# Optimization experiments

Measured on AMD Instinct MI355X. Metric: run time of the kernel, lower is better.

The kernel has to match this reference:

```python
import jax, jax.numpy as jnp
import numpy as np

B, T, H, OUT, L = 125, 512, 512, 1024, 2


def _rnn_layer(xs, w_ih, w_hh, b_ih, b_hh):
    # xs: [B, T, H_in] -> scan over time with tanh recurrence
    xs_t = jnp.swapaxes(xs, 0, 1)  # [T, B, H_in]
    h0 = jnp.zeros((xs.shape[0], w_hh.shape[0]), dtype=xs.dtype)

    def step(h, x_t):
        h = jnp.tanh(x_t @ w_ih.T + b_ih + h @ w_hh.T + b_hh)
        return h, h

    h_last, hs = jax.lax.scan(step, h0, xs_t)
    return jnp.swapaxes(hs, 0, 1), h_last  # [B, T, H], [B, H]


def setup_inputs() -> dict:
    key = jax.random.key(0)
    ks = jax.random.split(key, 8)
    s = 1.0 / np.sqrt(H)
    x = jax.random.normal(ks[0], (B, T, H), dtype=jnp.float32)
    w_ih = jax.random.uniform(ks[1], (L, H, H), jnp.float32, -s, s)
    w_hh = jax.random.uniform(ks[2], (L, H, H), jnp.float32, -s, s)
    b_ih = jax.random.uniform(ks[3], (L, H), jnp.float32, -s, s)
    b_hh = jax.random.uniform(ks[4], (L, H), jnp.float32, -s, s)
    fc_w = jax.random.uniform(ks[5], (OUT, H), jnp.float32, -s, s)
    fc_b = jax.random.uniform(ks[6], (OUT,), jnp.float32, -s, s)
    return {"x": x, "w_ih": w_ih, "w_hh": w_hh, "b_ih": b_ih,
            "b_hh": b_hh, "fc_w": fc_w, "fc_b": fc_b}


def reference(x, w_ih, w_hh, b_ih, b_hh, fc_w, fc_b):
    h = x
    finals = []
    for l in range(L):  # small fixed layer loop
        h, h_last = _rnn_layer(h, w_ih[l], w_hh[l], b_ih[l], b_hh[l])
        finals.append(h_last)
    hidden = jnp.stack(finals, axis=0)  # [L, B, H]
    out = h.reshape(-1, H) @ fc_w.T + fc_b  # [B*T, OUT]
    return out, hidden
```

## Files before the change

kernel.cpp:

```cpp
#include <hip/hip_runtime.h>
#include <hip/hip_bf16.h>
#include <cstdint>

typedef short short8 __attribute__((ext_vector_type(8)));
typedef float f32x4 __attribute__((ext_vector_type(4)));
typedef uint32_t u32x2 __attribute__((ext_vector_type(2)));
typedef unsigned short u16;

#define DEVINL __device__ __forceinline__

DEVINL u16 f32_to_bf16(float f) {
  uint32_t u = __builtin_bit_cast(uint32_t, f);
  u += 0x7FFFu + ((u >> 16) & 1u);
  return (u16)(u >> 16);
}
DEVINL float bf16_to_f32(u16 b) {
  return __builtin_bit_cast(float, ((uint32_t)b) << 16);
}
DEVINL f32x4 mfma16(short8 a, short8 b, f32x4 c) {
  return __builtin_amdgcn_mfma_f32_16x16x32_bf16(a, b, c, 0, 0, 0);
}
DEVINL float tanh_e2(float x) {
  float e = __builtin_amdgcn_exp2f(x * 2.88539008177793f);
  return 1.f - __fdividef(2.f, 1.f + e);
}
DEVINL uint32_t cvt_pk_bf16(float lo, float hi) {
  uint32_t r;
  asm("v_cvt_pk_bf16_f32 %0, %1, %2" : "=v"(r) : "v"(lo), "v"(hi));
  return r;
}

__global__ void conv_bf16(const float* __restrict__ src, u16* __restrict__ dst, long n) {
  long i = ((long)blockIdx.x * blockDim.x + threadIdx.x) * 4;
  long stride = (long)gridDim.x * blockDim.x * 4;
  for (; i < n; i += stride) {
    float4 v = *(const float4*)(src + i);
    uint64_t p = (uint64_t)f32_to_bf16(v.x)
               | ((uint64_t)f32_to_bf16(v.y) << 16)
               | ((uint64_t)f32_to_bf16(v.z) << 32)
               | ((uint64_t)f32_to_bf16(v.w) << 48);
    *(uint64_t*)(dst + i) = p;
  }
}

__global__ void prep_bias(const float* __restrict__ bih, const float* __restrict__ bhh,
                          float* __restrict__ b1, float* __restrict__ b2) {
  int i = threadIdx.x;
  b1[i] = bih[i]       + bhh[i];
  b2[i] = bih[512 + i] + bhh[512 + i];
}

DEVINL void rec_window(char* LDS, int g, const u16* __restrict__ Whh,
                       const u16* __restrict__ U, u16* __restrict__ Hout,
                       float* __restrict__ hidden, u16* __restrict__ hstate, int win) {
  const int tid  = threadIdx.x;
  const int lane = tid & 63;
  const int w    = tid >> 6;
  const int q    = lane >> 4;
  const int r16  = lane & 15;
  const int t0   = win << 6;

  short8 wreg[3][16];
#pragma unroll
  for (int tt = 0; tt < 3; ++tt)
#pragma unroll
    for (int kk = 0; kk < 16; ++kk)
      wreg[tt][kk] = *(const short8*)(Whh + (size_t)(w * 64 + tt * 16 + r16) * 512 + kk * 32 + q * 8);

#pragma unroll
  for (int kk = 0; kk < 16; ++kk) {
    short8 v = *(const short8*)(Whh + (size_t)(w * 64 + 48 + r16) * 512 + kk * 32 + q * 8);
    *(short8*)(LDS + w * 16384 + kk * 1024 + q * 256 + r16 * 16) = v;
  }

  if (win == 0) {
    short8 z = {0, 0, 0, 0, 0, 0, 0, 0};
    *(short8*)(LDS + 131072 + tid * 32)      = z;
    *(short8*)(LDS + 131072 + tid * 32 + 16) = z;
  } else {
    short8 a = *(const short8*)(hstate + (size_t)g * 8192 + tid * 16);
    short8 b = *(const short8*)(hstate + (size_t)g * 8192 + tid * 16 + 8);
    *(short8*)(LDS + 131072 + tid * 32)      = a;
    *(short8*)(LDS + 131072 + tid * 32 + 16) = b;
  }

  uint32_t rd  = 131072 + q * 256 + r16 * 16;
  uint32_t wrb = 147456 + w * 2048 + (q >> 1) * 256 + r16 * 16 + (q & 1) * 8;
  const uint32_t wlb = w * 16384 + q * 256 + r16 * 16;
  const int jb = w * 64 + q * 4;
  const char* Ub = (const char*)U;
  const uint32_t ubase = (uint32_t)(g * 512 + tid) * 32;
  char* Hc = (char*)Hout;
  uint32_t hoff = (uint32_t)(g * 16 + r16) * 524288u + (uint32_t)jb * 2u + (uint32_t)t0 * 1024u;

  short8 u  = *(const short8*)(Ub + ubase + (uint32_t)t0 * 131072u);
  short8 u2 = *(const short8*)(Ub + ubase + (uint32_t)t0 * 131072u + 16);
  __syncthreads();

  for (int t = t0; t < t0 + 64; ++t) {
    f32x4 D0, D1, D2, D3;
#pragma unroll
    for (int rg = 0; rg < 4; ++rg) {
      D0[rg] = bf16_to_f32((u16)u[rg]);
      D1[rg] = bf16_to_f32((u16)u[rg + 4]);
      D2[rg] = bf16_to_f32((u16)u2[rg]);
      D3[rg] = bf16_to_f32((u16)u2[rg + 4]);
    }
    {
      uint32_t off = ubase + (uint32_t)((t + 1 <= 511) ? (t + 1) : 511) * 131072u;
      u  = *(const short8*)(Ub + off);
      u2 = *(const short8*)(Ub + off + 16);
    }
#pragma unroll
    for (int kk = 0; kk < 16; ++kk) {
      short8 hf = *(const short8*)(LDS + rd + kk * 1024);
      short8 wl = *(const short8*)(LDS + wlb + kk * 1024);
      D0 = mfma16(wreg[0][kk], hf, D0);
      D1 = mfma16(wreg[1][kk], hf, D1);
      D2 = mfma16(wreg[2][kk], hf, D2);
      D3 = mfma16(wl, hf, D3);
    }
#define EPI_TILE(Dt, tt) { \
    float e0 = tanh_e2(Dt[0]), e1 = tanh_e2(Dt[1]); \
    float e2 = tanh_e2(Dt[2]), e3 = tanh_e2(Dt[3]); \
    u32x2 pk; pk[0] = cvt_pk_bf16(e0, e1); pk[1] = cvt_pk_bf16(e2, e3); \
    *(u32x2*)(LDS + wrb + ((tt) >> 1) * 1024 + ((tt) & 1) * 512) = pk; \
    *(u32x2*)(Hc + hoff + (tt) * 32) = pk; \
  }
    EPI_TILE(D0, 0); EPI_TILE(D1, 1); EPI_TILE(D2, 2); EPI_TILE(D3, 3);
#undef EPI_TILE
    hoff += 1024;

    rd ^= 16384; wrb ^= 16384;
    asm volatile("s_waitcnt lgkmcnt(0)" ::: "memory");
    __builtin_amdgcn_s_barrier();
    asm volatile("" ::: "memory");
  }

  {
    short8 a = *(const short8*)(LDS + 131072 + tid * 32);
    short8 b = *(const short8*)(LDS + 131072 + tid * 32 + 16);
    *(short8*)(hstate + (size_t)g * 8192 + tid * 16)     = a;
    *(short8*)(hstate + (size_t)g * 8192 + tid * 16 + 8) = b;
  }

  if (win == 7) {
    int b = g * 16 + r16;
    if (b < 125) {
      uint32_t fwr = 131072 + w * 2048 + (q >> 1) * 256 + r16 * 16 + (q & 1) * 8;
#pragma unroll
      for (int tt = 0; tt < 4; ++tt) {
        u32x2 pk = *(const u32x2*)(LDS + fwr + (tt >> 1) * 1024 + (tt & 1) * 512);
        float4 v;
        v.x = __builtin_bit_cast(float, pk[0] << 16);
        v.y = __builtin_bit_cast(float, pk[0] & 0xFFFF0000u);
        v.z = __builtin_bit_cast(float, pk[1] << 16);
        v.w = __builtin_bit_cast(float, pk[1] & 0xFFFF0000u);
        *(float4*)(hidden + (size_t)b * 512 + jb + tt * 16) = v;
      }
    }
  }
}

template <int MR, int AF32, int FRAG>
DEVINL void gemm_tile(char* LDS, const void* __restrict__ Ap,
                      const u16* __restrict__ B, const float* __restrict__ bias,
                      void* __restrict__ out, int brow, int bcol, int N) {
  u16* lA = (u16*)LDS;
  u16* lB = (u16*)(LDS + 16384);
  const int tid  = threadIdx.x;
  const int lane = tid & 63;
  const int wave = tid >> 6;
  const int wr = wave >> 2;
  const int wc = wave & 3;
  const int q   = lane >> 4;
  const int r16 = lane & 15;
  const int MT = MR / 32;

  f32x4 acc[MT][2];
#pragma unroll
  for (int i = 0; i < MT; ++i)
#pragma unroll
    for (int j = 0; j < 2; ++j) acc[i][j] = (f32x4){0.f, 0.f, 0.f, 0.f};

  for (int kt = 0; kt < 8; ++kt) {
    if (AF32) {
#pragma unroll
      for (int s = 0; s < 2; ++s) {
        int c   = tid * 2 + s;
        int row = c >> 3;
        int seg = c & 7;
        const float* src = (const float*)Ap + (size_t)(brow + row) * 512 + kt * 64 + seg * 8;
        float4 a0 = *(const float4*)(src);
        float4 a1 = *(const float4*)(src + 4);
        u32x2 p0, p1;
        p0[0] = cvt_pk_bf16(a0.x, a0.y); p0[1] = cvt_pk_bf16(a0.z, a0.w);
        p1[0] = cvt_pk_bf16(a1.x, a1.y); p1[1] = cvt_pk_bf16(a1.z, a1.w);
        int dsw = (seg * 16) ^ ((row & 7) << 4);
        *(u32x2*)((char*)lA + row * 128 + dsw)     = p0;
        *(u32x2*)((char*)lA + row * 128 + (dsw ^ 8)) = p1;
      }
    } else {
      const int CH = MR / 64;
#pragma unroll
      for (int s = 0; s < CH; ++s) {
        int c   = tid * CH + s;
        int row = c >> 3;
        int cb  = (c & 7) * 16;
        int dsw = cb ^ ((row & 7) << 4);
        short8 va = *(const short8*)((const u16*)Ap + (size_t)(brow + row) * 512 + kt * 64 + (cb >> 1));
        *(short8*)((char*)lA + row * 128 + dsw) = va;
      }
    }
#pragma unroll
    for (int s = 0; s < 2; ++s) {
      int c   = tid * 2 + s;
      int row = c >> 3;
      int cb  = (c & 7) * 16;
      int dsw = cb ^ ((row & 7) << 4);
      short8 vb = *(const short8*)(B + (size_t)(bcol + row) * 512 + kt * 64 + (cb >> 1));
      *(short8*)((char*)lB + row * 128 + dsw) = vb;
    }
    __syncthreads();
#pragma unroll
    for (int kk = 0; kk < 2; ++kk) {
      short8 af[MT], bfr[2];
#pragma unroll
      for (int mt = 0; mt < MT; ++mt) {
        int row = wr * (MR / 2) + mt * 16 + r16;
        int byt = (kk * 64 + q * 16) ^ ((row & 7) << 4);
        af[mt] = *(const short8*)((const char*)lA + row * 128 + byt);
      }
#pragma unroll
      for (int nt = 0; nt < 2; ++nt) {
        int row = wc * 32 + nt * 16 + r16;
        int byt = (kk * 64 + q * 16) ^ ((row & 7) << 4);
        bfr[nt] = *(const short8*)((const char*)lB + row * 128 + byt);
      }
#pragma unroll
      for (int mt = 0; mt < MT; ++mt)
#pragma unroll
        for (int nt = 0; nt < 2; ++nt)
          acc[mt][nt] = mfma16(af[mt], bfr[nt], acc[mt][nt]);
    }
    __syncthreads();
  }

#pragma unroll
  for (int mt = 0; mt < MT; ++mt) {
#pragma unroll
    for (int nt = 0; nt < 2; ++nt) {
      int jc = bcol + wc * 32 + nt * 16 + r16;
      float bv = bias[jc];
      if (!FRAG) {
#pragma unroll
        for (int rg = 0; rg < 4; ++rg) {
          int mg = brow + wr * (MR / 2) + mt * 16 + q * 4 + rg;
          ((float*)out)[(size_t)mg * N + jc] = acc[mt][nt][rg] + bv;
        }
      } else {
        int tidc    = (jc >> 6) * 64 + ((jc >> 2) & 3) * 16;
        int colpart = ((jc >> 4) & 3) * 4 + (jc & 3);
#pragma unroll
        for (int rg = 0; rg < 4; ++rg) {
          int mg = brow + wr * (MR / 2) + mt * 16 + q * 4 + rg;
          int bb = mg >> 9;
          int t2 = mg & 511;
          size_t idx = (((size_t)t2 * 8 + (bb >> 4)) * 512 + tidc + (bb & 15)) * 16 + colpart;
          ((u16*)out)[idx] = f32_to_bf16(acc[mt][nt][rg] + bv);
        }
      }
    }
  }
}

__attribute__((amdgpu_flat_work_group_size(512, 512), amdgpu_waves_per_eu(2, 2)))
__global__ void phase(const u16* __restrict__ Whh1, const u16* __restrict__ Whh2,
                      u16* __restrict__ U1, u16* __restrict__ U2,
                      u16* __restrict__ H1, u16* __restrict__ H2,
                      u16* __restrict__ hs1, u16* __restrict__ hs2,
                      const float* __restrict__ Xf, const u16* __restrict__ Wih1,
                      const u16* __restrict__ Wih2, const u16* __restrict__ FCW,
                      const float* __restrict__ b1, const float* __restrict__ b2,
                      const float* __restrict__ fcb,
                      float* __restrict__ outp, float* __restrict__ hid,
                      int rec1w, int rec2w, int njobs, int j0, int j1, int j2, int j3) {
  __shared__ char LDS[163840];
  const int bx = blockIdx.x;
  if (bx < 8) {
    if (rec1w >= 0) rec_window(LDS, bx, Whh1, U1, H1, hid, hs1, rec1w);
  } else if (bx < 16) {
    if (rec2w >= 0) rec_window(LDS, bx - 8, Whh2, U2, H2, hid + 64000, hs2, rec2w);
  } else if (njobs > 0) {
    const int widx = bx - 16;
    int jobs[4] = {j0, j1, j2, j3};
    int cnt[4], total = 0;
    for (int i = 0; i < njobs; ++i) { cnt[i] = ((jobs[i] >> 4) == 2) ? 1000 : 500; total += cnt[i]; }
    for (int tile = widx; tile < total; tile += 240) {
      int rem = tile, jj = 0;
      while (jj < njobs - 1 && rem >= cnt[jj]) { rem -= cnt[jj]; ++jj; }
      int kind = jobs[jj] >> 4, wn = jobs[jj] & 15;
      if (kind == 0)
        gemm_tile<128, 1, 1>(LDS, Xf, Wih1, b1, U1,
                             (rem >> 2) * 512 + wn * 128, (rem & 3) * 128, 512);
      else if (kind == 1)
        gemm_tile<64, 0, 1>(LDS, H1, Wih2, b2, U2,
                            (rem >> 2) * 512 + wn * 64, (rem & 3) * 128, 512);
      else
        gemm_tile<128, 0, 0>(LDS, H2, FCW, fcb, outp,
                             (rem >> 3) * 512 + wn * 128, (rem & 7) * 128, 1024);
    }
  }
}

#define J(k, w) ((k) * 16 + (w))

extern "C" void kernel_launch(void* const* d_in, const int* in_sizes, int n_in,
                              void* d_out, int out_size, void* d_ws, size_t ws_size,
                              hipStream_t stream) {
  const float* x   = (const float*)d_in[0];
  const float* wih = (const float*)d_in[1];
  const float* whh = (const float*)d_in[2];
  const float* bih = (const float*)d_in[3];
  const float* bhh = (const float*)d_in[4];
  const float* fcw = (const float*)d_in[5];
  const float* fcb = (const float*)d_in[6];

  char* ws = (char*)d_ws;
  float* outp = (float*)d_out;
  float* hid  = outp + 65536000;
  u16*   U1   = (u16*)d_out;

  u16* Wih1 = (u16*)(ws + 0);
  u16* Whh1 = (u16*)(ws + 524288);
  u16* Wih2 = (u16*)(ws + 1048576);
  u16* Whh2 = (u16*)(ws + 1572864);
  u16* FCW  = (u16*)(ws + 2097152);
  float* b1 = (float*)(ws + 3145728);
  float* b2 = b1 + 512;
  u16* hs1  = (u16*)(ws + 3276800);
  u16* hs2  = (u16*)(ws + 3407872);

  conv_bf16<<<256, 256, 0, stream>>>(wih,          Wih1, 262144L);
  conv_bf16<<<256, 256, 0, stream>>>(wih + 262144, Wih2, 262144L);
  conv_bf16<<<256, 256, 0, stream>>>(whh,          Whh1, 262144L);
  conv_bf16<<<256, 256, 0, stream>>>(whh + 262144, Whh2, 262144L);
  conv_bf16<<<512, 256, 0, stream>>>(fcw, FCW, 524288L);
  prep_bias<<<1, 512, 0, stream>>>(bih, bhh, b1, b2);

  if (ws_size >= 205520896ull) {
    u16* U2 = (u16*)(ws + 4194304);
    u16* H1 = (u16*)(ws + 71303168);
    u16* H2 = (u16*)(ws + 138412032);
#define PH(r1, r2, nj, a, b, c, d) \
    phase<<<256, 512, 0, stream>>>(Whh1, Whh2, U1, U2, H1, H2, hs1, hs2, x, \
                                   Wih1, Wih2, FCW, b1, b2, fcb, outp, hid, \
                                   r1, r2, nj, a, b, c, d)
    PH(-1, -1, 1, J(0,0), 0, 0, 0);
    PH( 0, -1, 3, J(0,1), J(0,2), J(0,3), 0);
    PH( 1, -1, 1, J(1,0), 0, 0, 0);
    PH( 2,  0, 1, J(1,1), 0, 0, 0);
    PH( 3,  1, 1, J(1,2), 0, 0, 0);
    PH( 4,  2, 1, J(1,3), 0, 0, 0);
    PH( 5,  3, 1, J(1,4), 0, 0, 0);
    PH( 6,  4, 1, J(1,5), 0, 0, 0);
    PH( 7,  5, 1, J(1,6), 0, 0, 0);
    PH(-1,  6, 3, J(1,7), J(2,0), J(2,1), 0);
    PH(-1,  7, 1, J(2,2), 0, 0, 0);
    PH(-1, -1, 1, J(2,3), 0, 0, 0);
#undef PH
  } else {
    u16* U2 = U1;
    u16* H1 = (u16*)(ws + 4194304);
    u16* H2 = H1;
#define PH(r1, r2, nj, a, b, c, d) \
    phase<<<256, 512, 0, stream>>>(Whh1, Whh2, U1, U2, H1, H2, hs1, hs2, x, \
                                   Wih1, Wih2, FCW, b1, b2, fcb, outp, hid, \
                                   r1, r2, nj, a, b, c, d)
    PH(-1, -1, 4, J(0,0), J(0,1), J(0,2), J(0,3));
    for (int w = 0; w < 8; ++w) PH(w, -1, 0, 0, 0, 0, 0);
    PH(-1, -1, 4, J(1,0), J(1,1), J(1,2), J(1,3));
    PH(-1, -1, 4, J(1,4), J(1,5), J(1,6), J(1,7));
    for (int w = 0; w < 8; ++w) PH(-1, w, 0, 0, 0, 0, 0);
    PH(-1, -1, 2, J(2,0), J(2,1), 0, 0);
    PH(-1, -1, 2, J(2,2), J(2,3), 0, 0);
#undef PH
  }

  (void)in_sizes; (void)n_in; (void)out_size;
}
```

Baseline: 1.720 ms.

## Pair row-tiles sharing B in layer-2 and FC GEMMs, fuse prep kernels

Replaces the templated GEMM tile with a dedicated float-input version for layer 1 and a paired version for the layer-2 input projection and the FC GEMM. The paired version loads one B tile and computes two 64-row A tiles from different batch blocks against it, so B traffic is shared. The FC GEMM is now split into 8 row windows instead of 4, rescheduling it across the last phases to better overlap with the layer-2 recurrence. The six weight/bias prep launches are merged into one kernel to cut launch overhead.

```diff
diff --git a/kernel.cpp b/kernel.cpp
--- a/kernel.cpp
+++ b/kernel.cpp
@@ -30,24 +30,34 @@
   return r;
 }
 
-__global__ void conv_bf16(const float* __restrict__ src, u16* __restrict__ dst, long n) {
-  long i = ((long)blockIdx.x * blockDim.x + threadIdx.x) * 4;
-  long stride = (long)gridDim.x * blockDim.x * 4;
-  for (; i < n; i += stride) {
-    float4 v = *(const float4*)(src + i);
-    uint64_t p = (uint64_t)f32_to_bf16(v.x)
-               | ((uint64_t)f32_to_bf16(v.y) << 16)
-               | ((uint64_t)f32_to_bf16(v.z) << 32)
-               | ((uint64_t)f32_to_bf16(v.w) << 48);
-    *(uint64_t*)(dst + i) = p;
-  }
-}
-
-__global__ void prep_bias(const float* __restrict__ bih, const float* __restrict__ bhh,
-                          float* __restrict__ b1, float* __restrict__ b2) {
-  int i = threadIdx.x;
-  b1[i] = bih[i]       + bhh[i];
-  b2[i] = bih[512 + i] + bhh[512 + i];
+__global__ void conv_all(const float* __restrict__ wih, const float* __restrict__ whh,
+                         const float* __restrict__ fcw, const float* __restrict__ bih,
+                         const float* __restrict__ bhh,
+                         u16* __restrict__ Wih1, u16* __restrict__ Wih2,
+                         u16* __restrict__ Whh1, u16* __restrict__ Whh2,
+                         u16* __restrict__ FCW, float* __restrict__ b1,
+                         float* __restrict__ b2) {
+  const int bx = blockIdx.x, tid = threadIdx.x;
+  if (bx == 1536) {
+    for (int i = tid; i < 512; i += 256) {
+      b1[i] = bih[i]       + bhh[i];
+      b2[i] = bih[512 + i] + bhh[512 + i];
+    }
+    return;
+  }
+  const float* src; u16* dst; int off;
+  if (bx < 256)       { src = wih;          dst = Wih1; off = bx; }
+  else if (bx < 512)  { src = wih + 262144; dst = Wih2; off = bx - 256; }
+  else if (bx < 768)  { src = whh;          dst = Whh1; off = bx - 512; }
+  else if (bx < 1024) { src = whh + 262144; dst = Whh2; off = bx - 768; }
+  else                { src = fcw;          dst = FCW;  off = bx - 1024; }
+  long i = (long)off * 1024 + tid * 4;
+  float4 v = *(const float4*)(src + i);
+  uint64_t p = (uint64_t)f32_to_bf16(v.x)
+             | ((uint64_t)f32_to_bf16(v.y) << 16)
+             | ((uint64_t)f32_to_bf16(v.z) << 32)
+             | ((uint64_t)f32_to_bf16(v.w) << 48);
+  *(uint64_t*)(dst + i) = p;
 }
 
 DEVINL void rec_window(char* LDS, int g, const u16* __restrict__ Whh,
@@ -162,10 +172,9 @@
   }
 }
 
-template <int MR, int AF32, int FRAG>
-DEVINL void gemm_tile(char* LDS, const void* __restrict__ Ap,
-                      const u16* __restrict__ B, const float* __restrict__ bias,
-                      void* __restrict__ out, int brow, int bcol, int N) {
+DEVINL void gemm_g1(char* LDS, const float* __restrict__ Ap, const u16* __restrict__ B,
+                    const float* __restrict__ bias, u16* __restrict__ out,
+                    int brow, int bcol) {
   u16* lA = (u16*)LDS;
   u16* lB = (u16*)(LDS + 16384);
   const int tid  = threadIdx.x;
@@ -175,42 +184,28 @@
   const int wc = wave & 3;
   const int q   = lane >> 4;
   const int r16 = lane & 15;
-  const int MT = MR / 32;
-
-  f32x4 acc[MT][2];
-#pragma unroll
-  for (int i = 0; i < MT; ++i)
+
+  f32x4 acc[4][2];
+#pragma unroll
+  for (int i = 0; i < 4; ++i)
 #pragma unroll
     for (int j = 0; j < 2; ++j) acc[i][j] = (f32x4){0.f, 0.f, 0.f, 0.f};
 
   for (int kt = 0; kt < 8; ++kt) {
-    if (AF32) {
-#pragma unroll
-      for (int s = 0; s < 2; ++s) {
-        int c   = tid * 2 + s;
-        int row = c >> 3;
-        int seg = c & 7;
-        const float* src = (const float*)Ap + (size_t)(brow + row) * 512 + kt * 64 + seg * 8;
-        float4 a0 = *(const float4*)(src);
-        float4 a1 = *(const float4*)(src + 4);
-        u32x2 p0, p1;
-        p0[0] = cvt_pk_bf16(a0.x, a0.y); p0[1] = cvt_pk_bf16(a0.z, a0.w);
-        p1[0] = cvt_pk_bf16(a1.x, a1.y); p1[1] = cvt_pk_bf16(a1.z, a1.w);
-        int dsw = (seg * 16) ^ ((row & 7) << 4);
-        *(u32x2*)((char*)lA + row * 128 + dsw)     = p0;
-        *(u32x2*)((char*)lA + row * 128 + (dsw ^ 8)) = p1;
-      }
-    } else {
-      const int CH = MR / 64;
-#pragma unroll
-      for (int s = 0; s < CH; ++s) {
-        int c   = tid * CH + s;
-        int row = c >> 3;
-        int cb  = (c & 7) * 16;
-        int dsw = cb ^ ((row & 7) << 4);
-        short8 va = *(const short8*)((const u16*)Ap + (size_t)(brow + row) * 512 + kt * 64 + (cb >> 1));
-        *(short8*)((char*)lA + row * 128 + dsw) = va;
-      }
+#pragma unroll
+    for (int s = 0; s < 2; ++s) {
+      int c   = tid * 2 + s;
+      int row = c >> 3;
+      int seg = c & 7;
+      const float* src = Ap + (size_t)(brow + row) * 512 + kt * 64 + seg * 8;
+      float4 a0 = *(const float4*)(src);
+      float4 a1 = *(const float4*)(src + 4);
+      u32x2 p0, p1;
+      p0[0] = cvt_pk_bf16(a0.x, a0.y); p0[1] = cvt_pk_bf16(a0.z, a0.w);
+      p1[0] = cvt_pk_bf16(a1.x, a1.y); p1[1] = cvt_pk_bf16(a1.z, a1.w);
+      int dsw = (seg * 16) ^ ((row & 7) << 4);
+      *(u32x2*)((char*)lA + row * 128 + dsw)       = p0;
+      *(u32x2*)((char*)lA + row * 128 + (dsw ^ 8)) = p1;
     }
 #pragma unroll
     for (int s = 0; s < 2; ++s) {
@@ -224,10 +219,10 @@
     __syncthreads();
 #pragma unroll
     for (int kk = 0; kk < 2; ++kk) {
-      short8 af[MT], bfr[2];
-#pragma unroll
-      for (int mt = 0; mt < MT; ++mt) {
-        int row = wr * (MR / 2) + mt * 16 + r16;
+      short8 af[4], bfr[2];
+#pragma unroll
+      for (int mt = 0; mt < 4; ++mt) {
+        int row = wr * 64 + mt * 16 + r16;
         int byt = (kk * 64 + q * 16) ^ ((row & 7) << 4);
         af[mt] = *(const short8*)((const char*)lA + row * 128 + byt);
       }
@@ -238,7 +233,7 @@
         bfr[nt] = *(const short8*)((const char*)lB + row * 128 + byt);
       }
 #pragma unroll
-      for (int mt = 0; mt < MT; ++mt)
+      for (int mt = 0; mt < 4; ++mt)
 #pragma unroll
         for (int nt = 0; nt < 2; ++nt)
           acc[mt][nt] = mfma16(af[mt], bfr[nt], acc[mt][nt]);
@@ -247,31 +242,129 @@
   }
 
 #pragma unroll
-  for (int mt = 0; mt < MT; ++mt) {
+  for (int mt = 0; mt < 4; ++mt) {
 #pragma unroll
     for (int nt = 0; nt < 2; ++nt) {
       int jc = bcol + wc * 32 + nt * 16 + r16;
       float bv = bias[jc];
-      if (!FRAG) {
-#pragma unroll
-        for (int rg = 0; rg < 4; ++rg) {
-          int mg = brow + wr * (MR / 2) + mt * 16 + q * 4 + rg;
-          ((float*)out)[(size_t)mg * N + jc] = acc[mt][nt][rg] + bv;
+      int tidc    = (jc >> 6) * 64 + ((jc >> 2) & 3) * 16;
+      int colpart = ((jc >> 4) & 3) * 4 + (jc & 3);
+#pragma unroll
+      for (int rg = 0; rg < 4; ++rg) {
+        int mg = brow + wr * 64 + mt * 16 + q * 4 + rg;
+        int bb = mg >> 9;
+        int t2 = mg & 511;
+        size_t idx = (((size_t)t2 * 8 + (bb >> 4)) * 512 + tidc + (bb & 15)) * 16 + colpart;
+        out[idx] = f32_to_bf16(acc[mt][nt][rg] + bv);
+      }
+    }
+  }
+}
+
+template <int FRAG>
+DEVINL void gemm_pair(char* LDS, const u16* __restrict__ Ap, int brow0, int brow1,
+                      const u16* __restrict__ B, const float* __restrict__ bias,
+                      void* __restrict__ out, int bcol, int N) {
+  u16* lB  = (u16*)LDS;
+  u16* lA0 = (u16*)(LDS + 16384);
+  u16* lA1 = (u16*)(LDS + 24576);
+  const int tid  = threadIdx.x;
+  const int lane = tid & 63;
+  const int wave = tid >> 6;
+  const int wr = wave >> 2;
+  const int wc = wave & 3;
+  const int q   = lane >> 4;
+  const int r16 = lane & 15;
+
+  f32x4 acc0[2][2], acc1[2][2];
+#pragma unroll
+  for (int i = 0; i < 2; ++i)
+#pragma unroll
+    for (int j = 0; j < 2; ++j) {
+      acc0[i][j] = (f32x4){0.f, 0.f, 0.f, 0.f};
+      acc1[i][j] = (f32x4){0.f, 0.f, 0.f, 0.f};
+    }
+
+  for (int kt = 0; kt < 8; ++kt) {
+#pragma unroll
+    for (int s = 0; s < 2; ++s) {
+      int c   = tid * 2 + s;
+      int row = c >> 3;
+      int cb  = (c & 7) * 16;
+      int dsw = cb ^ ((row & 7) << 4);
+      short8 vb = *(const short8*)(B + (size_t)(bcol + row) * 512 + kt * 64 + (cb >> 1));
+      *(short8*)((char*)lB + row * 128 + dsw) = vb;
+    }
+    {
+      int row = tid >> 3;
+      int cb  = (tid & 7) * 16;
+      int dsw = cb ^ ((row & 7) << 4);
+      short8 va = *(const short8*)(Ap + (size_t)(brow0 + row) * 512 + kt * 64 + (cb >> 1));
+      *(short8*)((char*)lA0 + row * 128 + dsw) = va;
+      if (brow1 >= 0) {
+        short8 vc = *(const short8*)(Ap + (size_t)(brow1 + row) * 512 + kt * 64 + (cb >> 1));
+        *(short8*)((char*)lA1 + row * 128 + dsw) = vc;
+      }
+    }
+    __syncthreads();
+#pragma unroll
+    for (int kk = 0; kk < 2; ++kk) {
+      short8 bfr[2];
+#pragma unroll
+      for (int nt = 0; nt < 2; ++nt) {
+        int row = wc * 32 + nt * 16 + r16;
+        int byt = (kk * 64 + q * 16) ^ ((row & 7) << 4);
+        bfr[nt] = *(const short8*)((const char*)lB + row * 128 + byt);
+      }
+#pragma unroll
+      for (int mt = 0; mt < 2; ++mt) {
+        int row = wr * 32 + mt * 16 + r16;
+        int byt = (kk * 64 + q * 16) ^ ((row & 7) << 4);
+        short8 a0 = *(const short8*)((const char*)lA0 + row * 128 + byt);
+#pragma unroll
+        for (int nt = 0; nt < 2; ++nt)
+          acc0[mt][nt] = mfma16(a0, bfr[nt], acc0[mt][nt]);
+        if (brow1 >= 0) {
+          short8 a1 = *(const short8*)((const char*)lA1 + row * 128 + byt);
+#pragma unroll
+          for (int nt = 0; nt < 2; ++nt)
+            acc1[mt][nt] = mfma16(a1, bfr[nt], acc1[mt][nt]);
         }
-      } else {
-        int tidc    = (jc >> 6) * 64 + ((jc >> 2) & 3) * 16;
-        int colpart = ((jc >> 4) & 3) * 4 + (jc & 3);
-#pragma unroll
-        for (int rg = 0; rg < 4; ++rg) {
-          int mg = brow + wr * (MR / 2) + mt * 16 + q * 4 + rg;
-          int bb = mg >> 9;
-          int t2 = mg & 511;
-          size_t idx = (((size_t)t2 * 8 + (bb >> 4)) * 512 + tidc + (bb & 15)) * 16 + colpart;
-          ((u16*)out)[idx] = f32_to_bf16(acc[mt][nt][rg] + bv);
-        }
-      }
-    }
-  }
+      }
+    }
+    __syncthreads();
+  }
+
+#define EPI_PAIR(ACC, BROW) { \
+  _Pragma("unroll") \
+  for (int mt = 0; mt < 2; ++mt) { \
+    _Pragma("unroll") \
+    for (int nt = 0; nt < 2; ++nt) { \
+      int jc = bcol + wc * 32 + nt * 16 + r16; \
+      float bv = bias[jc]; \
+      if (!FRAG) { \
+        _Pragma("unroll") \
+        for (int rg = 0; rg < 4; ++rg) { \
+          int mg = (BROW) + wr * 32 + mt * 16 + q * 4 + rg; \
+          ((float*)out)[(size_t)mg * N + jc] = ACC[mt][nt][rg] + bv; \
+        } \
+      } else { \
+        int tidc    = (jc >> 6) * 64 + ((jc >> 2) & 3) * 16; \
+        int colpart = ((jc >> 4) & 3) * 4 + (jc & 3); \
+        _Pragma("unroll") \
+        for (int rg = 0; rg < 4; ++rg) { \
+          int mg = (BROW) + wr * 32 + mt * 16 + q * 4 + rg; \
+          int bb = mg >> 9; \
+          int t2 = mg & 511; \
+          size_t idx = (((size_t)t2 * 8 + (bb >> 4)) * 512 + tidc + (bb & 15)) * 16 + colpart; \
+          ((u16*)out)[idx] = f32_to_bf16(ACC[mt][nt][rg] + bv); \
+        } \
+      } \
+    } \
+  } }
+  EPI_PAIR(acc0, brow0);
+  if (brow1 >= 0) EPI_PAIR(acc1, brow1);
+#undef EPI_PAIR
 }
 
 __attribute__((amdgpu_flat_work_group_size(512, 512), amdgpu_waves_per_eu(2, 2)))
@@ -284,7 +377,8 @@
                       const float* __restrict__ b1, const float* __restrict__ b2,
                       const float* __restrict__ fcb,
                       float* __restrict__ outp, float* __restrict__ hid,
-                      int rec1w, int rec2w, int njobs, int j0, int j1, int j2, int j3) {
+                      int rec1w, int rec2w, int njobs,
+                      int j0, int j1, int j2, int j3, int j4) {
   __shared__ char LDS[163840];
   const int bx = blockIdx.x;
   if (bx < 8) {
@@ -293,22 +387,30 @@
     if (rec2w >= 0) rec_window(LDS, bx - 8, Whh2, U2, H2, hid + 64000, hs2, rec2w);
   } else if (njobs > 0) {
     const int widx = bx - 16;
-    int jobs[4] = {j0, j1, j2, j3};
-    int cnt[4], total = 0;
-    for (int i = 0; i < njobs; ++i) { cnt[i] = ((jobs[i] >> 4) == 2) ? 1000 : 500; total += cnt[i]; }
+    int jobs[5] = {j0, j1, j2, j3, j4};
+    int cnt[5], total = 0;
+    for (int i = 0; i < njobs; ++i) {
+      int k = jobs[i] >> 4;
+      cnt[i] = (k == 0) ? 500 : (k == 1) ? 252 : 504;
+      total += cnt[i];
+    }
     for (int tile = widx; tile < total; tile += 240) {
       int rem = tile, jj = 0;
       while (jj < njobs - 1 && rem >= cnt[jj]) { rem -= cnt[jj]; ++jj; }
       int kind = jobs[jj] >> 4, wn = jobs[jj] & 15;
-      if (kind == 0)
-        gemm_tile<128, 1, 1>(LDS, Xf, Wih1, b1, U1,
-                             (rem >> 2) * 512 + wn * 128, (rem & 3) * 128, 512);
-      else if (kind == 1)
-        gemm_tile<64, 0, 1>(LDS, H1, Wih2, b2, U2,
-                            (rem >> 2) * 512 + wn * 64, (rem & 3) * 128, 512);
-      else
-        gemm_tile<128, 0, 0>(LDS, H2, FCW, fcb, outp,
-                             (rem >> 3) * 512 + wn * 128, (rem & 7) * 128, 1024);
+      if (kind == 0) {
+        gemm_g1(LDS, Xf, Wih1, b1, U1, (rem >> 2) * 512 + wn * 128, (rem & 3) * 128);
+      } else if (kind == 1) {
+        int n = rem & 3, p = rem >> 2;
+        int m0 = 2 * p, m1 = (p == 62) ? -1 : m0 + 1;
+        gemm_pair<1>(LDS, H1, m0 * 512 + wn * 64, (m1 < 0) ? -1 : m1 * 512 + wn * 64,
+                     Wih2, b2, U2, n * 128, 512);
+      } else {
+        int n = rem & 7, p = rem >> 3;
+        int m0 = 2 * p, m1 = (p == 62) ? -1 : m0 + 1;
+        gemm_pair<0>(LDS, H2, m0 * 512 + wn * 64, (m1 < 0) ? -1 : m1 * 512 + wn * 64,
+                     FCW, fcb, outp, n * 128, 1024);
+      }
     }
   }
 }
@@ -341,49 +443,45 @@
   u16* hs1  = (u16*)(ws + 3276800);
   u16* hs2  = (u16*)(ws + 3407872);
 
-  conv_bf16<<<256, 256, 0, stream>>>(wih,          Wih1, 262144L);
-  conv_bf16<<<256, 256, 0, stream>>>(wih + 262144, Wih2, 262144L);
-  conv_bf16<<<256, 256, 0, stream>>>(whh,          Whh1, 262144L);
-  conv_bf16<<<256, 256, 0, stream>>>(whh + 262144, Whh2, 262144L);
-  conv_bf16<<<512, 256, 0, stream>>>(fcw, FCW, 524288L);
-  prep_bias<<<1, 512, 0, stream>>>(bih, bhh, b1, b2);
+  conv_all<<<1537, 256, 0, stream>>>(wih, whh, fcw, bih, bhh,
+                                     Wih1, Wih2, Whh1, Whh2, FCW, b1, b2);
 
   if (ws_size >= 205520896ull) {
     u16* U2 = (u16*)(ws + 4194304);
     u16* H1 = (u16*)(ws + 71303168);
     u16* H2 = (u16*)(ws + 138412032);
-#define PH(r1, r2, nj, a, b, c, d) \
+#define PH(r1, r2, nj, a, b, c, d, e) \
     phase<<<256, 512, 0, stream>>>(Whh1, Whh2, U1, U2, H1, H2, hs1, hs2, x, \
                                    Wih1, Wih2, FCW, b1, b2, fcb, outp, hid, \
-                                   r1, r2, nj, a, b, c, d)
-    PH(-1, -1, 1, J(0,0), 0, 0, 0);
-    PH( 0, -1, 3, J(0,1), J(0,2), J(0,3), 0);
-    PH( 1, -1, 1, J(1,0), 0, 0, 0);
-    PH( 2,  0, 1, J(1,1), 0, 0, 0);
-    PH( 3,  1, 1, J(1,2), 0, 0, 0);
-    PH( 4,  2, 1, J(1,3), 0, 0, 0);
-    PH( 5,  3, 1, J(1,4), 0, 0, 0);
-    PH( 6,  4, 1, J(1,5), 0, 0, 0);
-    PH( 7,  5, 1, J(1,6), 0, 0, 0);
-    PH(-1,  6, 3, J(1,7), J(2,0), J(2,1), 0);
-    PH(-1,  7, 1, J(2,2), 0, 0, 0);
-    PH(-1, -1, 1, J(2,3), 0, 0, 0);
+                                   r1, r2, nj, a, b, c, d, e)
+    PH(-1, -1, 1, J(0,0), 0, 0, 0, 0);
+    PH( 0, -1, 3, J(0,1), J(0,2), J(0,3), 0, 0);
+    PH( 1, -1, 1, J(1,0), 0, 0, 0, 0);
+    PH( 2,  0, 1, J(1,1), 0, 0, 0, 0);
+    PH( 3,  1, 1, J(1,2), 0, 0, 0, 0);
+    PH( 4,  2, 1, J(1,3), 0, 0, 0, 0);
+    PH( 5,  3, 1, J(1,4), 0, 0, 0, 0);
+    PH( 6,  4, 1, J(1,5), 0, 0, 0, 0);
+    PH( 7,  5, 1, J(1,6), 0, 0, 0, 0);
+    PH(-1,  6, 5, J(1,7), J(2,0), J(2,1), J(2,2), J(2,3));
+    PH(-1,  7, 3, J(2,4), J(2,5), J(2,6), 0, 0);
+    PH(-1, -1, 1, J(2,7), 0, 0, 0, 0);
 #undef PH
   } else {
     u16* U2 = U1;
     u16* H1 = (u16*)(ws + 4194304);
     u16* H2 = H1;
-#define PH(r1, r2, nj, a, b, c, d) \
+#define PH(r1, r2, nj, a, b, c, d, e) \
     phase<<<256, 512, 0, stream>>>(Whh1, Whh2, U1, U2, H1, H2, hs1, hs2, x, \
                                    Wih1, Wih2, FCW, b1, b2, fcb, outp, hid, \
-                                   r1, r2, nj, a, b, c, d)
-    PH(-1, -1, 4, J(0,0), J(0,1), J(0,2), J(0,3));
-    for (int w = 0; w < 8; ++w) PH(w, -1, 0, 0, 0, 0, 0);
-    PH(-1, -1, 4, J(1,0), J(1,1), J(1,2), J(1,3));
-    PH(-1, -1, 4, J(1,4), J(1,5), J(1,6), J(1,7));
-    for (int w = 0; w < 8; ++w) PH(-1, w, 0, 0, 0, 0, 0);
-    PH(-1, -1, 2, J(2,0), J(2,1), 0, 0);
-    PH(-1, -1, 2, J(2,2), J(2,3), 0, 0);
+                                   r1, r2, nj, a, b, c, d, e)
+    PH(-1, -1, 4, J(0,0), J(0,1), J(0,2), J(0,3), 0);
+    for (int w = 0; w < 8; ++w) PH(w, -1, 0, 0, 0, 0, 0, 0);
+    PH(-1, -1, 4, J(1,0), J(1,1), J(1,2), J(1,3), 0);
+    PH(-1, -1, 4, J(1,4), J(1,5), J(1,6), J(1,7), 0);
+    for (int w = 0; w < 8; ++w) PH(-1, w, 0, 0, 0, 0, 0, 0);
+    PH(-1, -1, 4, J(2,0), J(2,1), J(2,2), J(2,3), 0);
+    PH(-1, -1, 4, J(2,4), J(2,5), J(2,6), J(2,7), 0);
 #undef PH
   }
 
```

Result: no change. 1.687 ms (-1.9%).
